# Kernel optimization log

Measured on AMD Instinct MI355X. Metric: run time of the kernel, lower is better.

Reference implementation:

```python
import jax, jax.numpy as jnp
import numpy as np

EPS = 1e-5
NUM_HEADS = 20


def ln(x, w, b=None):
    m = x.mean(-1, keepdims=True)
    v = x.var(-1, keepdims=True)
    y = (x - m) * jax.lax.rsqrt(v + EPS) * w
    return y + b if b is not None else y


def rotate_half(t):
    t1, t2 = jnp.split(t, 2, axis=-1)
    return jnp.concatenate([-t2, t1], axis=-1)


def setup_inputs() -> dict:
    key = jax.random.key(0)
    B, S, E = 8, 1024, 1280  # 8 packed sequences of length 1024, ESM-2 650M width
    T = B * S
    ks = jax.random.split(key, 6)
    scale = (1.0 / E) ** 0.5  # ~xavier scale
    w = lambda k: jax.random.normal(k, (E, E), jnp.float32) * scale
    return {
        "x": jax.random.normal(ks[0], (T, E), jnp.float32),
        "cu_lens": jnp.arange(B + 1, dtype=jnp.int32) * S,
        "max_len": S,
        "norm_w": jnp.ones((E,), jnp.float32),
        "norm_b": jnp.zeros((E,), jnp.float32),
        "Wq": w(ks[1]),
        "Wk": w(ks[2]),
        "Wv": w(ks[3]),
        "Wout": w(ks[4]),
        "lnq_w": jnp.ones((E,), jnp.float32),
        "lnk_w": jnp.ones((E,), jnp.float32),
    }


def reference(x, cu_lens, max_len, norm_w, norm_b, Wq, Wk, Wv, Wout, lnq_w, lnk_w):
    T, E = x.shape
    H = NUM_HEADS
    D = E // H

    # pre-norm + separate Q/K/V projections (bias=False)
    h = ln(x, norm_w, norm_b)
    q = ln(h @ Wq.T, lnq_w)   # per-head-stack LayerNorm on q (no bias)
    k = ln(h @ Wk.T, lnk_w)
    v = h @ Wv.T

    q = q.reshape(T, H, D)
    k = k.reshape(T, H, D)
    v = v.reshape(T, H, D)

    # rotary embedding: positions restart at each sequence boundary (cu_lens)
    tok = jnp.arange(T)
    seg = jnp.searchsorted(cu_lens, tok, side="right") - 1
    pos = (tok - cu_lens[seg]).astype(jnp.float32)
    inv_freq = 1.0 / (10000.0 ** (jnp.arange(0, D, 2, dtype=jnp.float32) / D))
    f = pos[:, None] * inv_freq[None, :]                      # [T, D/2]
    cos = jnp.concatenate([jnp.cos(f), jnp.cos(f)], -1)[:, None, :]  # [T,1,D]
    sin = jnp.concatenate([jnp.sin(f), jnp.sin(f)], -1)[:, None, :]
    q = q * cos + rotate_half(q) * sin
    k = k * cos + rotate_half(k) * sin

    # varlen flash attention; sequences are equal-length here so reshape to
    # [B,S,...] which exactly honors the block-diagonal (no cross-sequence) mask
    B = cu_lens.shape[0] - 1
    S = T // B
    qb = q.reshape(B, S, H, D)
    kb = k.reshape(B, S, H, D)
    vb = v.reshape(B, S, H, D)

    scores = jnp.einsum("bqhd,bkhd->bhqk", qb, kb) * (D ** -0.5)
    attn = jax.nn.softmax(scores, axis=-1)
    o = jnp.einsum("bhqk,bkhd->bqhd", attn, vb).reshape(T, E)
    return o @ Wout.T
```

## Files before the change

### kernel.cpp

```cpp
#include <hip/hip_runtime.h>
#include <hip/hip_bf16.h>
#include <math.h>

#define NH 20
#define HD 64
#define E_DIM 1280
#define T_TOK 8192
#define NSEQ 8
#define N4 (E_DIM * E_DIM / 4)

#define SCALE_LOG2 0.1803368801111204f

typedef unsigned short u16;
typedef unsigned int u32;
typedef __attribute__((ext_vector_type(8))) short bf16x8;
typedef __attribute__((ext_vector_type(4))) float f32x4;
typedef __attribute__((ext_vector_type(16))) float f32x16;

__device__ __forceinline__ float bf2f(u16 h) {
  union { float f; unsigned u; } c; c.u = ((unsigned)h) << 16; return c.f;
}
__device__ __forceinline__ u16 f2bf(float f) {
  union { float f; unsigned u; } c; c.f = f;
  unsigned u = c.u;
  return (u16)((u + 0x7fffu + ((u >> 16) & 1u)) >> 16);
}
__device__ __forceinline__ u32 cvtpk(float lo, float hi) {
  u32 r;
  asm("v_cvt_pk_bf16_f32 %0, %1, %2" : "=v"(r) : "v"(lo), "v"(hi));
  return r;
}

__device__ __forceinline__ void gld_lds16(const void* g, void* l) {
  __builtin_amdgcn_global_load_lds((const __attribute__((address_space(1))) void*)g,
                                   (__attribute__((address_space(3))) void*)l,
                                   16, 0, 0);
}

#define BARR() __builtin_amdgcn_s_barrier()
#define LGKM0() do { asm volatile("s_waitcnt lgkmcnt(0)" ::: "memory"); \
                     __builtin_amdgcn_sched_barrier(0); } while (0)
#define VMC4() asm volatile("s_waitcnt vmcnt(4)" ::: "memory")
#define VMC0() asm volatile("s_waitcnt vmcnt(0)" ::: "memory")

__global__ __launch_bounds__(256) void cvt_all(const float* __restrict__ Wq,
                                               const float* __restrict__ Wk,
                                               const float* __restrict__ Wv,
                                               const float* __restrict__ Wo,
                                               u16* __restrict__ wqkv,
                                               u16* __restrict__ wo) {
  int i = blockIdx.x * 256 + threadIdx.x;
  if (i >= 4 * N4) return;
  int r = i / N4;
  int l = i - r * N4;
  const float* src = (r == 0) ? Wq : (r == 1) ? Wk : (r == 2) ? Wv : Wo;
  float4 v = ((const float4*)src)[l];
  ushort4 ov;
  ov.x = f2bf(v.x); ov.y = f2bf(v.y); ov.z = f2bf(v.z); ov.w = f2bf(v.w);
  if (r < 3) ((ushort4*)wqkv)[(size_t)r * N4 + l] = ov;
  else       ((ushort4*)wo)[l] = ov;
}

__global__ __launch_bounds__(256) void rope_tab_kernel(float2* __restrict__ tab) {
  int i = blockIdx.x * 256 + threadIdx.x;
  if (i >= 1024 * 32) return;
  int pos = i >> 5, dm = i & 31;
  float freq = exp2f(-(float)dm * (13.287712379549449f / 32.0f));
  float f = (float)pos * freq;
  tab[i] = make_float2(cosf(f), sinf(f));
}

__global__ __launch_bounds__(320) void ln_x_kernel(const float* __restrict__ x,
                                                   const float* __restrict__ w,
                                                   const float* __restrict__ b,
                                                   u16* __restrict__ h) {
  const int row = blockIdx.x;
  const int tid = threadIdx.x;
  const float4 xv = ((const float4*)(x + (size_t)row * E_DIM))[tid];
  float s  = xv.x + xv.y + xv.z + xv.w;
  float s2 = xv.x*xv.x + xv.y*xv.y + xv.z*xv.z + xv.w*xv.w;
#pragma unroll
  for (int m = 1; m < 64; m <<= 1) { s += __shfl_xor(s, m); s2 += __shfl_xor(s2, m); }
  __shared__ float ss[5], ss2[5];
  if ((tid & 63) == 0) { ss[tid >> 6] = s; ss2[tid >> 6] = s2; }
  __syncthreads();
  s  = ss[0] + ss[1] + ss[2] + ss[3] + ss[4];
  s2 = ss2[0] + ss2[1] + ss2[2] + ss2[3] + ss2[4];
  const float mean = s * (1.0f / E_DIM);
  const float var  = s2 * (1.0f / E_DIM) - mean * mean;
  const float rstd = rsqrtf(var + 1e-5f);
  const float4 wv = ((const float4*)w)[tid];
  const float4 bv = ((const float4*)b)[tid];
  ushort4 o;
  o.x = f2bf((xv.x - mean) * rstd * wv.x + bv.x);
  o.y = f2bf((xv.y - mean) * rstd * wv.y + bv.y);
  o.z = f2bf((xv.z - mean) * rstd * wv.z + bv.z);
  o.w = f2bf((xv.w - mean) * rstd * wv.w + bv.w);
  ((ushort4*)(h + (size_t)row * E_DIM))[tid] = o;
}

__global__ __launch_bounds__(320) void ln_rope2_kernel(const u16* __restrict__ preq,
                                                       const u16* __restrict__ prek,
                                                       const float* __restrict__ wq,
                                                       const float* __restrict__ wk,
                                                       const int* __restrict__ cu,
                                                       const float2* __restrict__ tab,
                                                       u16* __restrict__ outq,
                                                       u16* __restrict__ outk) {
  const int sel = blockIdx.x >> 13;
  const int row = blockIdx.x & (T_TOK - 1);
  const u16* pre = sel ? prek : preq;
  const float* w = sel ? wk : wq;
  u16* outp = sel ? outk : outq;
  const float oscale = sel ? 1.0f : SCALE_LOG2;
  const int tid = threadIdx.x;
  __shared__ float y[E_DIM];
  const ushort4 qv = ((const ushort4*)(pre + (size_t)row * E_DIM))[tid];
  float v0 = bf2f(qv.x), v1 = bf2f(qv.y), v2 = bf2f(qv.z), v3 = bf2f(qv.w);
  float s  = v0 + v1 + v2 + v3;
  float s2 = v0*v0 + v1*v1 + v2*v2 + v3*v3;
#pragma unroll
  for (int m = 1; m < 64; m <<= 1) { s += __shfl_xor(s, m); s2 += __shfl_xor(s2, m); }
  __shared__ float ss[5], ss2[5];
  if ((tid & 63) == 0) { ss[tid >> 6] = s; ss2[tid >> 6] = s2; }
  __syncthreads();
  s  = ss[0] + ss[1] + ss[2] + ss[3] + ss[4];
  s2 = ss2[0] + ss2[1] + ss2[2] + ss2[3] + ss2[4];
  const float mean = s * (1.0f / E_DIM);
  const float var  = s2 * (1.0f / E_DIM) - mean * mean;
  const float rstd = rsqrtf(var + 1e-5f);
  const int e0 = tid * 4;
  float4 wv = ((const float4*)w)[tid];
  wv.x *= oscale; wv.y *= oscale; wv.z *= oscale; wv.w *= oscale;
  y[e0 + 0] = (v0 - mean) * rstd * wv.x;
  y[e0 + 1] = (v1 - mean) * rstd * wv.y;
  y[e0 + 2] = (v2 - mean) * rstd * wv.z;
  y[e0 + 3] = (v3 - mean) * rstd * wv.w;
  __syncthreads();
  int seg = 0;
#pragma unroll
  for (int bb = 1; bb < NSEQ + 1; bb++) if (cu[bb] <= row) seg = bb;
  const int pos = row - cu[seg];
  const int d0 = e0 & 63;
  const int hbase = e0 - d0;
  const float4* tp = (const float4*)(tab + pos * 32 + (d0 & 31));
  const float4 t0 = tp[0], t1 = tp[1];
  const float cs_[4] = {t0.x, t0.z, t1.x, t1.z};
  const float sn_[4] = {t0.y, t0.w, t1.y, t1.w};
  const bool lo = (d0 < 32);
  ushort4 o;
#pragma unroll
  for (int i = 0; i < 4; i++) {
    const int d = d0 + i;
    float r;
    if (lo) r = y[hbase + d] * cs_[i] - y[hbase + d + 32] * sn_[i];
    else    r = y[hbase + d] * cs_[i] + y[hbase + d - 32] * sn_[i];
    ((u16*)&o)[i] = f2bf(r);
  }
  ((ushort4*)(outp + (size_t)row * E_DIM))[tid] = o;
}

template <int MODE, int K>
__global__ __launch_bounds__(512) void gemm256(const u16* __restrict__ A,
                                               const u16* __restrict__ B,
                                               u16* __restrict__ preq,
                                               u16* __restrict__ prek,
                                               u16* __restrict__ vT,
                                               float* __restrict__ Cf) {
  __shared__ u16 As[2][16384];
  __shared__ u16 Bs[2][16384];
  const int tid = threadIdx.x;
  const int wid = tid >> 6, lane = tid & 63;
  const int l16 = lane & 15, lq = lane >> 4;
  const int wm = wid >> 2, wn = wid & 3;
  const int cpx = gridDim.x >> 3;
  const int bid = (blockIdx.x & 7) * cpx + (blockIdx.x >> 3);
  const int bm = bid & 31;
  const int bn = bid >> 5;
  const int m0 = bm << 8, n0 = bn << 8;
  const int sw = l16 & 7;

  const int row0 = tid >> 3;
  const int ch0 = ((tid & 7) ^ (row0 & 7)) << 3;
  const u16* Abase = A + (size_t)(m0 + row0) * K + ch0;
  const u16* Bbase = B + (size_t)(n0 + row0) * K + ch0;
  const int dst0 = tid * 8;

  const int CA = (wm * 128 + l16) * 64;
  const int CB = (wn * 64 + l16) * 64;
  const int ch_0 = ((0 | lq) ^ sw) << 3;
  const int ch_1 = ((4 | lq) ^ sw) << 3;

  f32x4 acc[8][4] = {};
  bf16x8 aF[4][2], bF[2][2][2];

#define STG(Larr, bufp, hh, gbase, kt) do {                                     \
    const u16* g_ = (gbase) + (size_t)(hh) * 128 * K + (size_t)(kt) * 64;       \
    gld_lds16(g_, &Larr[bufp][(hh) * 8192 + dst0]);                             \
    gld_lds16(g_ + (size_t)64 * K, &Larr[bufp][(hh) * 8192 + dst0 + 4096]);     \
  } while (0)

#define RDA(bufp, a) do {                                                       \
    _Pragma("unroll") for (int mb = 0; mb < 4; mb++) {                          \
      aF[mb][0] = *(const bf16x8*)(&As[bufp][CA + (a) * 4096 + mb * 1024 + ch_0]); \
      aF[mb][1] = *(const bf16x8*)(&As[bufp][CA + (a) * 4096 + mb * 1024 + ch_1]); \
    } } while (0)

#define RDB(bufp, b) do {                                                       \
    _Pragma("unroll") for (int nb = 0; nb < 2; nb++) {                          \
      bF[b][nb][0] = *(const bf16x8*)(&Bs[bufp][CB + (b) * 2048 + nb * 1024 + ch_0]); \
      bF[b][nb][1] = *(const bf16x8*)(&Bs[bufp][CB + (b) * 2048 + nb * 1024 + ch_1]); \
    } } while (0)

#define MFQ(a, b) do {                                                          \
    __builtin_amdgcn_s_setprio(1);                                              \
    _Pragma("unroll") for (int mb = 0; mb < 4; mb++)                            \
    _Pragma("unroll") for (int nb = 0; nb < 2; nb++)                            \
    _Pragma("unroll") for (int kk = 0; kk < 2; kk++)                            \
      acc[(a) * 4 + mb][(b) * 2 + nb] = __builtin_amdgcn_mfma_f32_16x16x32_bf16( \
          aF[mb][kk], bF[b][nb][kk], acc[(a) * 4 + mb][(b) * 2 + nb], 0, 0, 0); \
    __builtin_amdgcn_s_setprio(0); } while (0)

  STG(Bs, 0, 0, Bbase, 0);
  STG(As, 0, 0, Abase, 0);
  STG(Bs, 0, 1, Bbase, 0);
  STG(As, 0, 1, Abase, 0);
  STG(Bs, 1, 0, Bbase, 1);
  STG(As, 1, 0, Abase, 1);
  VMC4();
  BARR();

  const int NIT = K / 128;
  for (int i = 0; i < NIT; i++) {
    const bool lastI = (i == NIT - 1);
    const int k1 = 2 * i + 1, k2 = 2 * i + 2, k3 = 2 * i + 3;
    RDA(0, 0); RDB(0, 0);
    STG(Bs, 1, 1, Bbase, k1);
    LGKM0(); MFQ(0, 0); BARR();
    RDB(0, 1);
    STG(As, 1, 1, Abase, k1);
    LGKM0(); MFQ(0, 1); BARR();
    RDA(0, 1);
    if (!lastI) STG(Bs, 0, 0, Bbase, k2);
    LGKM0(); MFQ(1, 0); BARR();
    if (!lastI) STG(As, 0, 0, Abase, k2);
    LGKM0(); MFQ(1, 1);
    if (!lastI) VMC4(); else VMC0();
    BARR();
    RDA(1, 0); RDB(1, 0);
    if (!lastI) STG(Bs, 0, 1, Bbase, k2);
    LGKM0(); MFQ(0, 0); BARR();
    RDB(1, 1);
    if (!lastI) STG(As, 0, 1, Abase, k2);
    LGKM0(); MFQ(0, 1); BARR();
    RDA(1, 1);
    if (!lastI) STG(Bs, 1, 0, Bbase, k3);
    LGKM0(); MFQ(1, 0); BARR();
    if (!lastI) {
      STG(As, 1, 0, Abase, k3);
      LGKM0(); MFQ(1, 1);
      VMC4();
      BARR();
    } else {
      LGKM0(); MFQ(1, 1);
    }
  }
#undef STG
#undef RDA
#undef RDB
#undef MFQ

  if (MODE == 0) {
    if (n0 < 2560) {
      u16* dst; int c0;
      if (n0 < 1280) { dst = preq; c0 = n0; }
      else           { dst = prek; c0 = n0 - 1280; }
#pragma unroll
      for (int mi = 0; mi < 8; mi++)
#pragma unroll
        for (int j = 0; j < 4; j++) {
          const size_t rowo = (size_t)(m0 + wm * 128 + mi * 16 + lq * 4 + j) * E_DIM;
#pragma unroll
          for (int ni = 0; ni < 4; ni++)
            dst[rowo + c0 + wn * 64 + ni * 16 + l16] = f2bf(acc[mi][ni][j]);
        }
    } else {
      const int c0 = n0 - 2560;
#pragma unroll
      for (int mi = 0; mi < 8; mi++)
#pragma unroll
        for (int ni = 0; ni < 4; ni++) {
          ushort4 pkt;
          pkt.x = f2bf(acc[mi][ni][0]); pkt.y = f2bf(acc[mi][ni][1]);
          pkt.z = f2bf(acc[mi][ni][2]); pkt.w = f2bf(acc[mi][ni][3]);
          const size_t off = (size_t)(c0 + wn * 64 + ni * 16 + l16) * T_TOK +
                             (m0 + wm * 128 + mi * 16 + lq * 4);
          *(ushort4*)(vT + off) = pkt;
        }
    }
  } else {
#pragma unroll
    for (int mi = 0; mi < 8; mi++)
#pragma unroll
      for (int j = 0; j < 4; j++) {
        const size_t rowo = (size_t)(m0 + wm * 128 + mi * 16 + lq * 4 + j) * E_DIM;
#pragma unroll
        for (int ni = 0; ni < 4; ni++)
          Cf[rowo + n0 + wn * 64 + ni * 16 + l16] = acc[mi][ni][j];
      }
  }
}

__global__ __launch_bounds__(256) void attn_kernel(const u16* __restrict__ q,
                                                   const u16* __restrict__ k,
                                                   const u16* __restrict__ vT,
                                                   const int* __restrict__ cu,
                                                   u16* __restrict__ o) {
  const int bx = blockIdx.x;
  const int hb = bx % (NH * NSEQ);
  const int qt = bx / (NH * NSEQ);
  const int hh = hb % NH;
  const int b  = hb / NH;
  const int base = cu[b];
  const int nkt  = (cu[b + 1] - base) >> 6;
  const int tid  = threadIdx.x;
  const int wid  = tid >> 6, lane = tid & 63;
  const int l31  = lane & 31, hi = lane >> 5;

  __shared__ u16 Ks[2][64 * 64];
  __shared__ u16 Vs[2][64 * 64];

  const int qrow = base + qt * 128 + wid * 32 + l31;
  bf16x8 qf[4];
#pragma unroll
  for (int kk = 0; kk < 4; kk++)
    qf[kk] = *(const bf16x8*)(q + (size_t)qrow * E_DIM + hh * 64 + kk * 16 + hi * 8);

  f32x16 acc0 = {}, acc1 = {};
  float lrow = 0.f;

  const int r0 = tid >> 3;
  const int chs = tid & 7;
  const int cs0 = (chs ^ (r0 & 7)) << 3;
  const int r1 = r0 + 32;
  const int cs1 = (chs ^ (r1 & 7)) << 3;
  const u16* kg0 = k  + (size_t)(base + r0) * E_DIM + hh * 64 + cs0;
  const u16* kg1 = k  + (size_t)(base + r1) * E_DIM + hh * 64 + cs1;
  const u16* vg0 = vT + (size_t)(hh * 64 + r0) * T_TOK + base + cs0;
  const u16* vg1 = vT + (size_t)(hh * 64 + r1) * T_TOK + base + cs1;
  const int ldsoff = wid * 512;

  gld_lds16(kg0, &Ks[0][ldsoff]);
  gld_lds16(kg1, &Ks[0][2048 + ldsoff]);
  gld_lds16(vg0, &Vs[0][ldsoff]);
  gld_lds16(vg1, &Vs[0][2048 + ldsoff]);
  __syncthreads();

  int cur = 0;
  for (int kt = 0; kt < nkt; kt++) {
    if (kt + 1 < nkt) {
      const size_t ko = (size_t)(kt + 1) * 64 * E_DIM;
      const int vo = (kt + 1) * 64;
      u16* kd = Ks[cur ^ 1];
      u16* vd = Vs[cur ^ 1];
      gld_lds16(kg0 + ko, kd + ldsoff);
      gld_lds16(kg1 + ko, kd + 2048 + ldsoff);
      gld_lds16(vg0 + vo, vd + ldsoff);
      gld_lds16(vg1 + vo, vd + 2048 + ldsoff);
    }
    const u16* Kc = Ks[cur];
    const u16* Vc = Vs[cur];

    f32x16 S0 = {}, S1 = {};
#pragma unroll
    for (int kk = 0; kk < 4; kk++) {
      const int c0 = (((kk << 1) | hi) ^ (l31 & 7)) << 3;
      const bf16x8 kf0 = *(const bf16x8*)(Kc + l31 * 64 + c0);
      const bf16x8 kf1 = *(const bf16x8*)(Kc + (32 + l31) * 64 + c0);
      S0 = __builtin_amdgcn_mfma_f32_32x32x16_bf16(kf0, qf[kk], S0, 0, 0, 0);
      S1 = __builtin_amdgcn_mfma_f32_32x32x16_bf16(kf1, qf[kk], S1, 0, 0, 0);
    }

    float rs0 = 0.f, rs1 = 0.f, rs2 = 0.f, rs3 = 0.f;
#pragma unroll
    for (int r = 0; r < 16; r += 4) {
      S0[r + 0] = exp2f(S0[r + 0]); S0[r + 1] = exp2f(S0[r + 1]);
      S0[r + 2] = exp2f(S0[r + 2]); S0[r + 3] = exp2f(S0[r + 3]);
      rs0 += S0[r + 0]; rs1 += S0[r + 1]; rs2 += S0[r + 2]; rs3 += S0[r + 3];
    }
#pragma unroll
    for (int r = 0; r < 16; r += 4) {
      S1[r + 0] = exp2f(S1[r + 0]); S1[r + 1] = exp2f(S1[r + 1]);
      S1[r + 2] = exp2f(S1[r + 2]); S1[r + 3] = exp2f(S1[r + 3]);
      rs0 += S1[r + 0]; rs1 += S1[r + 1]; rs2 += S1[r + 2]; rs3 += S1[r + 3];
    }
    float rs = (rs0 + rs1) + (rs2 + rs3);
    rs += __shfl_xor(rs, 32);
    lrow += rs;

    u32 pw[4][4];
#pragma unroll
    for (int ks = 0; ks < 4; ks++) {
      const int g = (ks & 1) << 3;
      u32 A0, A1, B0, B1;
      if (ks < 2) {
        A0 = cvtpk(S0[g + 0], S0[g + 1]); A1 = cvtpk(S0[g + 2], S0[g + 3]);
        B0 = cvtpk(S0[g + 4], S0[g + 5]); B1 = cvtpk(S0[g + 6], S0[g + 7]);
      } else {
        A0 = cvtpk(S1[g + 0], S1[g + 1]); A1 = cvtpk(S1[g + 2], S1[g + 3]);
        B0 = cvtpk(S1[g + 4], S1[g + 5]); B1 = cvtpk(S1[g + 6], S1[g + 7]);
      }
      asm("v_permlane32_swap_b32 %0, %1" : "+v"(A0), "+v"(B0));
      asm("v_permlane32_swap_b32 %0, %1" : "+v"(A1), "+v"(B1));
      pw[ks][0] = A0; pw[ks][1] = A1; pw[ks][2] = B0; pw[ks][3] = B1;
    }

#pragma unroll
    for (int ks = 0; ks < 4; ks++) {
      const bf16x8 pa = *(const bf16x8*)&pw[ks][0];
      const int c0 = (((ks << 1) | hi) ^ (l31 & 7)) << 3;
      const bf16x8 vf0 = *(const bf16x8*)(Vc + l31 * 64 + c0);
      const bf16x8 vf1 = *(const bf16x8*)(Vc + (32 + l31) * 64 + c0);
      acc0 = __builtin_amdgcn_mfma_f32_32x32x16_bf16(pa, vf0, acc0, 0, 0, 0);
      acc1 = __builtin_amdgcn_mfma_f32_32x32x16_bf16(pa, vf1, acc1, 0, 0, 0);
    }
    __syncthreads();
    cur ^= 1;
  }

  const float linv = 1.0f / lrow;
  const int tok0 = base + qt * 128 + wid * 32;
#pragma unroll
  for (int r = 0; r < 16; r++) {
    const int qr = (r & 3) + 8 * (r >> 2) + 4 * hi;
    const float ls = __shfl(linv, qr);
    const size_t ro = (size_t)(tok0 + qr) * E_DIM + hh * 64 + l31;
    o[ro]      = f2bf(acc0[r] * ls);
    o[ro + 32] = f2bf(acc1[r] * ls);
  }
}

extern "C" void kernel_launch(void* const* d_in, const int* in_sizes, int n_in,
                              void* d_out, int out_size, void* d_ws, size_t ws_size,
                              hipStream_t stream) {
  const float* x      = (const float*)d_in[0];
  const int*   cu     = (const int*)d_in[1];
  const float* norm_w = (const float*)d_in[3];
  const float* norm_b = (const float*)d_in[4];
  const float* Wq     = (const float*)d_in[5];
  const float* Wk     = (const float*)d_in[6];
  const float* Wv     = (const float*)d_in[7];
  const float* Wo     = (const float*)d_in[8];
  const float* lnq    = (const float*)d_in[9];
  const float* lnk    = (const float*)d_in[10];
  float* out = (float*)d_out;

  const size_t EE2 = (size_t)E_DIM * E_DIM * 2;
  const size_t TE2 = (size_t)T_TOK * E_DIM * 2;
  char* p = (char*)d_ws;
  u16* wqkv = (u16*)p; p += 3 * EE2;
  u16* wo_b = (u16*)p; p += EE2;
  u16* h_b  = (u16*)p; p += TE2;
  u16* preq = (u16*)p; p += TE2;
  u16* prek = (u16*)p; p += TE2;
  u16* vT_b = (u16*)p; p += TE2;
  float2* tab = (float2*)p; p += 1024 * 32 * sizeof(float2);

  cvt_all<<<(4 * N4 + 255) / 256, 256, 0, stream>>>(Wq, Wk, Wv, Wo, wqkv, wo_b);
  rope_tab_kernel<<<128, 256, 0, stream>>>(tab);
  ln_x_kernel<<<T_TOK, 320, 0, stream>>>(x, norm_w, norm_b, h_b);

  gemm256<0, E_DIM><<<480, 512, 0, stream>>>(h_b, wqkv, preq, prek, vT_b, nullptr);

  ln_rope2_kernel<<<2 * T_TOK, 320, 0, stream>>>(preq, prek, lnq, lnk, cu, tab, preq, prek);

  attn_kernel<<<8 * NH * NSEQ, 256, 0, stream>>>(preq, prek, vT_b, cu, h_b);

  gemm256<1, E_DIM><<<160, 512, 0, stream>>>(h_b, wo_b, nullptr, nullptr, nullptr, out);
}
```

Baseline: 265.0 us.

## Drop explicit LDS waits, move vmcnt waits earlier, remove XCD block remap in GEMM

Removes the explicit lgkmcnt(0) waits and sched_barriers before each MFMA group, so the compiler places LDS waits itself and can interleave more freely. The global-load waits become vmcnt(2) and move one phase earlier, ahead of the next stage's issue. The XCD-aware block index remapping is also dropped in favour of plain blockIdx ordering. The changes aim to cut stall time, but they risk LDS read/write hazards across barriers and worse L2 locality across XCDs.

```diff
diff --git a/kernel.cpp b/kernel.cpp
--- a/kernel.cpp
+++ b/kernel.cpp
@@ -38,8 +38,7 @@
 }
 
 #define BARR() __builtin_amdgcn_s_barrier()
-#define LGKM0() do { asm volatile("s_waitcnt lgkmcnt(0)" ::: "memory"); \
-                     __builtin_amdgcn_sched_barrier(0); } while (0)
+#define VMC2() asm volatile("s_waitcnt vmcnt(2)" ::: "memory")
 #define VMC4() asm volatile("s_waitcnt vmcnt(4)" ::: "memory")
 #define VMC0() asm volatile("s_waitcnt vmcnt(0)" ::: "memory")
 
@@ -173,10 +172,8 @@
   const int wid = tid >> 6, lane = tid & 63;
   const int l16 = lane & 15, lq = lane >> 4;
   const int wm = wid >> 2, wn = wid & 3;
-  const int cpx = gridDim.x >> 3;
-  const int bid = (blockIdx.x & 7) * cpx + (blockIdx.x >> 3);
-  const int bm = bid & 31;
-  const int bn = bid >> 5;
+  const int bm = blockIdx.x & 31;
+  const int bn = blockIdx.x >> 5;
   const int m0 = bm << 8, n0 = bn << 8;
   const int sw = l16 & 7;
 
@@ -236,33 +233,33 @@
     const int k1 = 2 * i + 1, k2 = 2 * i + 2, k3 = 2 * i + 3;
     RDA(0, 0); RDB(0, 0);
     STG(Bs, 1, 1, Bbase, k1);
-    LGKM0(); MFQ(0, 0); BARR();
+    MFQ(0, 0); BARR();
     RDB(0, 1);
     STG(As, 1, 1, Abase, k1);
-    LGKM0(); MFQ(0, 1); BARR();
+    MFQ(0, 1); BARR();
     RDA(0, 1);
     if (!lastI) STG(Bs, 0, 0, Bbase, k2);
-    LGKM0(); MFQ(1, 0); BARR();
+    MFQ(1, 0);
+    if (!lastI) VMC2(); else VMC0();
+    BARR();
     if (!lastI) STG(As, 0, 0, Abase, k2);
-    LGKM0(); MFQ(1, 1);
-    if (!lastI) VMC4(); else VMC0();
-    BARR();
+    MFQ(1, 1); BARR();
     RDA(1, 0); RDB(1, 0);
     if (!lastI) STG(Bs, 0, 1, Bbase, k2);
-    LGKM0(); MFQ(0, 0); BARR();
+    MFQ(0, 0); BARR();
     RDB(1, 1);
     if (!lastI) STG(As, 0, 1, Abase, k2);
-    LGKM0(); MFQ(0, 1); BARR();
+    MFQ(0, 1); BARR();
     RDA(1, 1);
     if (!lastI) STG(Bs, 1, 0, Bbase, k3);
-    LGKM0(); MFQ(1, 0); BARR();
+    MFQ(1, 0);
+    if (!lastI) VMC2();
+    BARR();
     if (!lastI) {
       STG(As, 1, 0, Abase, k3);
-      LGKM0(); MFQ(1, 1);
-      VMC4();
-      BARR();
+      MFQ(1, 1); BARR();
     } else {
-      LGKM0(); MFQ(1, 1);
+      MFQ(1, 1);
     }
   }
 #undef STG
```

After: 254.3 us. 4.0% less time.
